# Optimization experiments

Hardware: AMD Instinct MI355X
Metric: run time of the kernel (lower is better)

## Reference

```python
import jax, jax.numpy as jnp
import numpy as np

N, D = 16384, 128
T = 0.07  # temperature


def setup_inputs() -> dict:
    key = jax.random.key(0)
    x = jax.random.normal(key, (N, D), dtype=jnp.float32)
    # uniformity loss assumes unit-norm embeddings (else exp(||x||^2 / t) overflows)
    x = x / jnp.linalg.norm(x, axis=-1, keepdims=True)
    return {"x": x}


def reference(x):
    # x.matmul(x.T).div(t).exp().sum(-1).log().mean()
    sims = jnp.matmul(x, x.T) / T            # [N, N]
    return jnp.mean(jnp.log(jnp.sum(jnp.exp(sims), axis=-1)))
```

## Files before the change

kernel.cpp:

```cpp
#include <hip/hip_runtime.h>
#include <hip/hip_bf16.h>

#define NN 16384
#define DD 128
#define TS 64
#define NS 256
#define NTILES 32896
#define NB 2048
#define SQRT_SCALE 4.5398159622f

#define EXP_A 8388608.0f
#define EXP_K 1064986316.0f

typedef __attribute__((ext_vector_type(8))) short bf16x8;
typedef __attribute__((ext_vector_type(4))) float f32x4;

#define TRI(s) (256 * (s) - ((s) * ((s)-1)) / 2)

__global__ void convert_swz(const float* __restrict__ x, ushort* __restrict__ xb) {
    int t = blockIdx.x * blockDim.x + threadIdx.x;
    int r = t >> 4;
    int c = t & 15;
    const float4* src = (const float4*)(x + (size_t)r * DD + c * 8);
    float4 f0 = src[0];
    float4 f1 = src[1];
    float vals[8] = {f0.x, f0.y, f0.z, f0.w, f1.x, f1.y, f1.z, f1.w};
    bf16x8 v;
#pragma unroll
    for (int i = 0; i < 8; ++i) {
        __hip_bfloat16 h = __float2bfloat16(vals[i] * SQRT_SCALE);
        v[i] = (short)__builtin_bit_cast(unsigned short, h);
    }
    int cs = c ^ (r & 15);
    *(bf16x8*)(xb + (size_t)r * DD + cs * 8) = v;
}

__global__ __launch_bounds__(256, 3) void gemm_exp_tri(const ushort* __restrict__ xb,
                                                       float* __restrict__ rowsum,
                                                       ushort* __restrict__ colscr) {
    const int tid  = threadIdx.x;
    const int lane = tid & 63;
    const int cw   = tid >> 6;
    const int frow = lane & 15;
    const int kq   = lane >> 4;

    const int bid = blockIdx.x;
    const int R0 = (int)(((long long)bid * NTILES) >> 11);
    const int R1 = (int)(((long long)(bid + 1) * NTILES) >> 11);
    const int n  = R1 - R0;

    int s = (int)(256.5f - sqrtf(256.5f * 256.5f - 2.0f * (float)R0));
    if (s < 0) s = 0;
    if (s > 255) s = 255;
    while (s < 255 && TRI(s + 1) <= R0) ++s;
    while (s > 0 && TRI(s) > R0) --s;
    int ct = s + (R0 - TRI(s));

    int slot[4];
#pragma unroll
    for (int kk = 0; kk < 4; ++kk)
        slot[kk] = ((((kk << 2) | kq) ^ frow) << 3);

    const ushort* bbase = xb + (size_t)(cw * 16 + frow) * DD;

    auto bload = [&](bf16x8 (&buf)[4], int c) {
        const ushort* p = bbase + (size_t)c * (TS * DD);
#pragma unroll
        for (int kk = 0; kk < 4; ++kk)
            buf[kk] = *(const bf16x8*)(p + slot[kk]);
    };

    int ps = s, pc = ct;
    auto adv = [&]() { if (pc == 255) { ++ps; pc = ps; } else ++pc; };

    bf16x8 bA[4], bB[4];
    bload(bA, pc); adv();
    bload(bB, pc); adv();

    bf16x8 af[4][4];
    auto load_af = [&](int ss) {
#pragma unroll
        for (int m = 0; m < 4; ++m) {
            const ushort* p = xb + (size_t)(ss * TS + m * 16 + frow) * DD;
#pragma unroll
            for (int kk = 0; kk < 4; ++kk)
                af[m][kk] = *(const bf16x8*)(p + slot[kk]);
        }
    };
    load_af(s);

    const f32x4 zacc = {0.f, 0.f, 0.f, 0.f};
    float rs[4][4] = {};

    auto flush_rows = [&](int ss) {
#pragma unroll
        for (int m = 0; m < 4; ++m)
#pragma unroll
            for (int j = 0; j < 4; ++j) {
                float v = rs[m][j];
                v += __shfl_xor(v, 1);
                v += __shfl_xor(v, 2);
                v += __shfl_xor(v, 4);
                v += __shfl_xor(v, 8);
                rs[m][j] = v;
            }
        if (frow == 0) {
#pragma unroll
            for (int m = 0; m < 4; ++m)
#pragma unroll
                for (int j = 0; j < 4; ++j)
                    atomicAdd(&rowsum[ss * TS + m * 16 + kq * 4 + j], rs[m][j]);
        }
    };

    auto body = [&](bf16x8 (&buf)[4], int q) {
        f32x4 acc[4];
        __builtin_amdgcn_s_setprio(1);
#pragma unroll
        for (int kk = 0; kk < 4; ++kk) {
            if (kk == 0) {
#pragma unroll
                for (int m = 0; m < 4; ++m)
                    acc[m] = __builtin_amdgcn_mfma_f32_16x16x32_bf16(
                        af[m][0], buf[0], zacc, 0, 0, 0);
            } else {
#pragma unroll
                for (int m = 0; m < 4; ++m)
                    acc[m] = __builtin_amdgcn_mfma_f32_16x16x32_bf16(
                        af[m][kk], buf[kk], acc[m], 0, 0, 0);
            }
        }
        __builtin_amdgcn_s_setprio(0);

        if (q + 2 < n) { bload(buf, pc); adv(); }

        float cs = 0.f;
#pragma unroll
        for (int m = 0; m < 4; ++m)
#pragma unroll
            for (int j = 0; j < 4; ++j) {
                float b = __builtin_fmaf(acc[m][j], EXP_A, EXP_K);
                float e = __builtin_bit_cast(float, (int)b);
                rs[m][j] += e;
                cs += e;
            }
        ushort v = (ct == s) ? (ushort)0
                 : __builtin_bit_cast(ushort, __float2bfloat16(cs));
        colscr[(size_t)(R0 + q) * 256 + (cw << 6) + lane] = v;

        if (q + 1 < n) {
            int olds = s;
            if (ct == 255) { ++s; ct = s; } else ++ct;
            if (s != olds) {
                flush_rows(olds);
#pragma unroll
                for (int m = 0; m < 4; ++m)
#pragma unroll
                    for (int j = 0; j < 4; ++j)
                        rs[m][j] = 0.f;
                load_af(s);
            }
        }
    };

    for (int q = 0; q < n; q += 2) {
        body(bA, q);
        if (q + 1 < n) body(bB, q + 1);
    }

    flush_rows(s);
}

__global__ __launch_bounds__(256) void colreduce(const ushort* __restrict__ colscr,
                                                 float* __restrict__ rowsum) {
    const int k = blockIdx.x;
    const int p = k >> 1;
    const int h = k & 1;
    const int e = threadIdx.x;

    const int ctA = p, ctB = 255 - p;
    float aA = 0.f, aB = 0.f;
#pragma unroll 4
    for (int s = h; s <= ctA; s += 2) {
        int rank = TRI(s) + (ctA - s);
        aA += __bfloat162float(__builtin_bit_cast(__hip_bfloat16,
                  colscr[(size_t)rank * 256 + e]));
    }
#pragma unroll 4
    for (int s = h; s <= ctB; s += 2) {
        int rank = TRI(s) + (ctB - s);
        aB += __bfloat162float(__builtin_bit_cast(__hip_bfloat16,
                  colscr[(size_t)rank * 256 + e]));
    }

    __shared__ float pA[256], pB[256];
    pA[e] = aA; pB[e] = aB;
    __syncthreads();
    if (e < 64) {
        int base = (e >> 4) * 64 + (e & 15);
        float vA = pA[base] + pA[base + 16] + pA[base + 32] + pA[base + 48];
        float vB = pB[base] + pB[base + 16] + pB[base + 32] + pB[base + 48];
        atomicAdd(&rowsum[ctA * TS + e], vA);
        atomicAdd(&rowsum[ctB * TS + e], vB);
    }
}

__global__ void finalize_part(const float* __restrict__ rowsum,
                              float* __restrict__ partial) {
    const int tid = threadIdx.x;
    const int r = blockIdx.x * 256 + tid;
    float s = __builtin_amdgcn_logf(rowsum[r]) * 0.69314718056f;
#pragma unroll
    for (int o = 1; o < 64; o <<= 1)
        s += __shfl_xor(s, o);
    __shared__ float wsum[4];
    if ((tid & 63) == 0) wsum[tid >> 6] = s;
    __syncthreads();
    if (tid == 0)
        partial[blockIdx.x] = wsum[0] + wsum[1] + wsum[2] + wsum[3];
}

__global__ void finalize_sum(const float* __restrict__ partial, float* __restrict__ out) {
    float s = partial[threadIdx.x];
#pragma unroll
    for (int o = 1; o < 64; o <<= 1)
        s += __shfl_xor(s, o);
    if (threadIdx.x == 0)
        out[0] = s * (1.0f / NN);
}

extern "C" void kernel_launch(void* const* d_in, const int* in_sizes, int n_in,
                              void* d_out, int out_size, void* d_ws, size_t ws_size,
                              hipStream_t stream) {
    const float* x = (const float*)d_in[0];
    float* out = (float*)d_out;

    ushort* xb      = (ushort*)d_ws;
    float* rowsum   = (float*)((char*)d_ws + (size_t)NN * DD * 2);
    float* partial  = rowsum + NN;
    ushort* colscr  = (ushort*)(partial + 64);

    hipMemsetAsync(rowsum, 0, NN * sizeof(float), stream);
    convert_swz<<<(NN * 16) / 256, 256, 0, stream>>>(x, xb);
    gemm_exp_tri<<<NB, 256, 0, stream>>>(xb, rowsum, colscr);
    colreduce<<<256, 256, 0, stream>>>(colscr, rowsum);
    finalize_part<<<64, 256, 0, stream>>>(rowsum, partial);
    finalize_sum<<<1, 64, 0, stream>>>(partial, out);
}
```

Baseline: 92.93 us.

## Assign each block one row strip with column chunks; fuse column reduce with log finalize

The triangular GEMM+exp kernel now launches 16 blocks per row strip, and each block handles a contiguous chunk of that strip's column tiles. This removes the sqrt-based triangular index search and the mid-loop row flush and A reload, so each block does a single flush at the end. The column-reduction kernel is merged with the per-row log partial sum, which removes one launch. The trade-off is load imbalance: late strips give blocks very few tiles, and some blocks exit immediately. Each colfin block also now reduces its columns serially over all strips, with half as many blocks as before.

```diff
diff --git a/kernel.cpp b/kernel.cpp
--- a/kernel.cpp
+++ b/kernel.cpp
@@ -6,7 +6,6 @@
 #define TS 64
 #define NS 256
 #define NTILES 32896
-#define NB 2048
 #define SQRT_SCALE 4.5398159622f
 
 #define EXP_A 8388608.0f
@@ -44,17 +43,14 @@
     const int frow = lane & 15;
     const int kq   = lane >> 4;
 
-    const int bid = blockIdx.x;
-    const int R0 = (int)(((long long)bid * NTILES) >> 11);
-    const int R1 = (int)(((long long)(bid + 1) * NTILES) >> 11);
-    const int n  = R1 - R0;
-
-    int s = (int)(256.5f - sqrtf(256.5f * 256.5f - 2.0f * (float)R0));
-    if (s < 0) s = 0;
-    if (s > 255) s = 255;
-    while (s < 255 && TRI(s + 1) <= R0) ++s;
-    while (s > 0 && TRI(s) > R0) --s;
-    int ct = s + (R0 - TRI(s));
+    const int bidx = blockIdx.x;
+    const int s   = bidx >> 4;
+    const int c   = bidx & 15;
+    const int n_s = NS - s;
+    const int ct0 = s + ((c * n_s) >> 4);
+    const int ct1 = s + (((c + 1) * n_s) >> 4);
+    const int nt  = ct1 - ct0;
+    if (nt == 0) return;
 
     int slot[4];
 #pragma unroll
@@ -62,56 +58,29 @@
         slot[kk] = ((((kk << 2) | kq) ^ frow) << 3);
 
     const ushort* bbase = xb + (size_t)(cw * 16 + frow) * DD;
-
-    auto bload = [&](bf16x8 (&buf)[4], int c) {
-        const ushort* p = bbase + (size_t)c * (TS * DD);
+    auto bload = [&](bf16x8 (&buf)[4], int ct) {
+        const ushort* p = bbase + (size_t)ct * (TS * DD);
 #pragma unroll
         for (int kk = 0; kk < 4; ++kk)
             buf[kk] = *(const bf16x8*)(p + slot[kk]);
     };
 
-    int ps = s, pc = ct;
-    auto adv = [&]() { if (pc == 255) { ++ps; pc = ps; } else ++pc; };
-
     bf16x8 bA[4], bB[4];
-    bload(bA, pc); adv();
-    bload(bB, pc); adv();
+    bload(bA, ct0);
+    if (nt > 1) bload(bB, ct0 + 1);
 
     bf16x8 af[4][4];
-    auto load_af = [&](int ss) {
-#pragma unroll
-        for (int m = 0; m < 4; ++m) {
-            const ushort* p = xb + (size_t)(ss * TS + m * 16 + frow) * DD;
-#pragma unroll
-            for (int kk = 0; kk < 4; ++kk)
-                af[m][kk] = *(const bf16x8*)(p + slot[kk]);
-        }
-    };
-    load_af(s);
+#pragma unroll
+    for (int m = 0; m < 4; ++m) {
+        const ushort* p = xb + (size_t)(s * TS + m * 16 + frow) * DD;
+#pragma unroll
+        for (int kk = 0; kk < 4; ++kk)
+            af[m][kk] = *(const bf16x8*)(p + slot[kk]);
+    }
 
     const f32x4 zacc = {0.f, 0.f, 0.f, 0.f};
     float rs[4][4] = {};
-
-    auto flush_rows = [&](int ss) {
-#pragma unroll
-        for (int m = 0; m < 4; ++m)
-#pragma unroll
-            for (int j = 0; j < 4; ++j) {
-                float v = rs[m][j];
-                v += __shfl_xor(v, 1);
-                v += __shfl_xor(v, 2);
-                v += __shfl_xor(v, 4);
-                v += __shfl_xor(v, 8);
-                rs[m][j] = v;
-            }
-        if (frow == 0) {
-#pragma unroll
-            for (int m = 0; m < 4; ++m)
-#pragma unroll
-                for (int j = 0; j < 4; ++j)
-                    atomicAdd(&rowsum[ss * TS + m * 16 + kq * 4 + j], rs[m][j]);
-        }
-    };
+    size_t colidx = (size_t)(TRI(s) + (ct0 - s)) * 256 + (cw << 6) + lane;
 
     auto body = [&](bf16x8 (&buf)[4], int q) {
         f32x4 acc[4];
@@ -132,7 +101,7 @@
         }
         __builtin_amdgcn_s_setprio(0);
 
-        if (q + 2 < n) { bload(buf, pc); adv(); }
+        if (q + 2 < nt) bload(buf, ct0 + q + 2);
 
         float cs = 0.f;
 #pragma unroll
@@ -144,50 +113,52 @@
                 rs[m][j] += e;
                 cs += e;
             }
-        ushort v = (ct == s) ? (ushort)0
+        ushort v = (ct0 + q == s) ? (ushort)0
                  : __builtin_bit_cast(ushort, __float2bfloat16(cs));
-        colscr[(size_t)(R0 + q) * 256 + (cw << 6) + lane] = v;
-
-        if (q + 1 < n) {
-            int olds = s;
-            if (ct == 255) { ++s; ct = s; } else ++ct;
-            if (s != olds) {
-                flush_rows(olds);
-#pragma unroll
-                for (int m = 0; m < 4; ++m)
-#pragma unroll
-                    for (int j = 0; j < 4; ++j)
-                        rs[m][j] = 0.f;
-                load_af(s);
-            }
+        colscr[colidx + (size_t)q * 256] = v;
+    };
+
+    for (int q = 0; q < nt; q += 2) {
+        body(bA, q);
+        if (q + 1 < nt) body(bB, q + 1);
+    }
+
+#pragma unroll
+    for (int m = 0; m < 4; ++m)
+#pragma unroll
+        for (int j = 0; j < 4; ++j) {
+            float v = rs[m][j];
+            v += __shfl_xor(v, 1);
+            v += __shfl_xor(v, 2);
+            v += __shfl_xor(v, 4);
+            v += __shfl_xor(v, 8);
+            rs[m][j] = v;
         }
-    };
-
-    for (int q = 0; q < n; q += 2) {
-        body(bA, q);
-        if (q + 1 < n) body(bB, q + 1);
-    }
-
-    flush_rows(s);
-}
-
-__global__ __launch_bounds__(256) void colreduce(const ushort* __restrict__ colscr,
-                                                 float* __restrict__ rowsum) {
-    const int k = blockIdx.x;
-    const int p = k >> 1;
-    const int h = k & 1;
+    if (frow == 0) {
+#pragma unroll
+        for (int m = 0; m < 4; ++m)
+#pragma unroll
+            for (int j = 0; j < 4; ++j)
+                atomicAdd(&rowsum[s * TS + m * 16 + kq * 4 + j], rs[m][j]);
+    }
+}
+
+__global__ __launch_bounds__(256) void colfin(const ushort* __restrict__ colscr,
+                                              const float* __restrict__ rowsum,
+                                              float* __restrict__ partial) {
+    const int p = blockIdx.x;
     const int e = threadIdx.x;
-
     const int ctA = p, ctB = 255 - p;
+
     float aA = 0.f, aB = 0.f;
 #pragma unroll 4
-    for (int s = h; s <= ctA; s += 2) {
+    for (int s = 0; s <= ctA; ++s) {
         int rank = TRI(s) + (ctA - s);
         aA += __bfloat162float(__builtin_bit_cast(__hip_bfloat16,
                   colscr[(size_t)rank * 256 + e]));
     }
 #pragma unroll 4
-    for (int s = h; s <= ctB; s += 2) {
+    for (int s = 0; s <= ctB; ++s) {
         int rank = TRI(s) + (ctB - s);
         aB += __bfloat162float(__builtin_bit_cast(__hip_bfloat16,
                   colscr[(size_t)rank * 256 + e]));
@@ -196,36 +167,35 @@
     __shared__ float pA[256], pB[256];
     pA[e] = aA; pB[e] = aB;
     __syncthreads();
-    if (e < 64) {
-        int base = (e >> 4) * 64 + (e & 15);
-        float vA = pA[base] + pA[base + 16] + pA[base + 32] + pA[base + 48];
-        float vB = pB[base] + pB[base + 16] + pB[base + 32] + pB[base + 48];
-        atomicAdd(&rowsum[ctA * TS + e], vA);
-        atomicAdd(&rowsum[ctB * TS + e], vB);
-    }
-}
-
-__global__ void finalize_part(const float* __restrict__ rowsum,
-                              float* __restrict__ partial) {
-    const int tid = threadIdx.x;
-    const int r = blockIdx.x * 256 + tid;
-    float s = __builtin_amdgcn_logf(rowsum[r]) * 0.69314718056f;
+
+    float lsum = 0.f;
+    if (e < 128) {
+        const int half = e >> 6;
+        const int col  = e & 63;
+        const int base = (col >> 4) * 64 + (col & 15);
+        const float* P = half ? pB : pA;
+        float csum = P[base] + P[base + 16] + P[base + 32] + P[base + 48];
+        const int ct = half ? ctB : ctA;
+        float r = rowsum[ct * TS + col] + csum;
+        lsum = __builtin_amdgcn_logf(r) * 0.69314718056f;
+    }
+#pragma unroll
+    for (int o = 1; o < 64; o <<= 1)
+        lsum += __shfl_xor(lsum, o);
+    __shared__ float ws[4];
+    if ((e & 63) == 0) ws[e >> 6] = lsum;
+    __syncthreads();
+    if (e == 0)
+        partial[p] = ws[0] + ws[1] + ws[2] + ws[3];
+}
+
+__global__ void finalize_sum(const float* __restrict__ partial, float* __restrict__ out) {
+    const int t = threadIdx.x;
+    float s = partial[t] + partial[t + 64];
 #pragma unroll
     for (int o = 1; o < 64; o <<= 1)
         s += __shfl_xor(s, o);
-    __shared__ float wsum[4];
-    if ((tid & 63) == 0) wsum[tid >> 6] = s;
-    __syncthreads();
-    if (tid == 0)
-        partial[blockIdx.x] = wsum[0] + wsum[1] + wsum[2] + wsum[3];
-}
-
-__global__ void finalize_sum(const float* __restrict__ partial, float* __restrict__ out) {
-    float s = partial[threadIdx.x];
-#pragma unroll
-    for (int o = 1; o < 64; o <<= 1)
-        s += __shfl_xor(s, o);
-    if (threadIdx.x == 0)
+    if (t == 0)
         out[0] = s * (1.0f / NN);
 }
 
@@ -238,12 +208,11 @@
     ushort* xb      = (ushort*)d_ws;
     float* rowsum   = (float*)((char*)d_ws + (size_t)NN * DD * 2);
     float* partial  = rowsum + NN;
-    ushort* colscr  = (ushort*)(partial + 64);
+    ushort* colscr  = (ushort*)(partial + 128);
 
     hipMemsetAsync(rowsum, 0, NN * sizeof(float), stream);
     convert_swz<<<(NN * 16) / 256, 256, 0, stream>>>(x, xb);
-    gemm_exp_tri<<<NB, 256, 0, stream>>>(xb, rowsum, colscr);
-    colreduce<<<256, 256, 0, stream>>>(colscr, rowsum);
-    finalize_part<<<64, 256, 0, stream>>>(rowsum, partial);
+    gemm_exp_tri<<<NS * 16, 256, 0, stream>>>(xb, rowsum, colscr);
+    colfin<<<128, 256, 0, stream>>>(colscr, rowsum, partial);
     finalize_sum<<<1, 64, 0, stream>>>(partial, out);
 }
```

Measured after the change: 103.8 us. +11.7%, slower.
